# Kernel tuning notes

Hardware: AMD Instinct MI355X
Metric: run time of the kernel (lower is better)

The kernel has to match this reference:

```python
import jax, jax.numpy as jnp
import numpy as np

EMBED_DIM = 768
NUM_HEADS = 12
HEAD_DIM = EMBED_DIM // NUM_HEADS


def setup_inputs() -> dict:
    key = jax.random.key(0)
    k_x, k_wqkv, k_bqkv, k_wo, k_bo = jax.random.split(key, 5)
    B, S = 2, 4096
    x = jax.random.normal(k_x, (B, S, EMBED_DIM), dtype=jnp.float32)
    # nn.Linear default init: U(-1/sqrt(fan_in), 1/sqrt(fan_in))
    bound = 1.0 / np.sqrt(EMBED_DIM)
    w_qkv = jax.random.uniform(k_wqkv, (EMBED_DIM, 3 * EMBED_DIM), jnp.float32, -bound, bound)
    b_qkv = jax.random.uniform(k_bqkv, (3 * EMBED_DIM,), jnp.float32, -bound, bound)
    w_out = jax.random.uniform(k_wo, (EMBED_DIM, EMBED_DIM), jnp.float32, -bound, bound)
    b_out = jax.random.uniform(k_bo, (EMBED_DIM,), jnp.float32, -bound, bound)
    return {"x": x, "w_qkv": w_qkv, "b_qkv": b_qkv, "w_out": w_out, "b_out": b_out}


def reference(x, w_qkv, b_qkv, w_out, b_out):
    B, S, E = x.shape
    H, D = NUM_HEADS, HEAD_DIM
    qkv = x @ w_qkv + b_qkv                       # [B,S,3E]
    qkv = qkv.reshape(B, S, 3, H, D)
    q = qkv[:, :, 0].transpose(0, 2, 1, 3)        # [B,H,S,D]
    k = qkv[:, :, 1].transpose(0, 2, 1, 3)
    v = qkv[:, :, 2].transpose(0, 2, 1, 3)
    scores = jnp.einsum('bhqd,bhkd->bhqk', q, k) / jnp.sqrt(jnp.float32(D))
    causal = jnp.tril(jnp.ones((S, S), dtype=bool))
    scores = jnp.where(causal, scores, -jnp.inf)
    weights = jax.nn.softmax(scores, axis=-1)
    attended = jnp.einsum('bhqk,bhkd->bhqd', weights, v)  # [B,H,S,D]
    attended = attended.transpose(0, 2, 1, 3).reshape(B, S, E)
    return attended @ w_out + b_out
```

## Files before the change

kernel.cpp:

```cpp
#include <hip/hip_runtime.h>

#define EMBED 768
#define NH 12
#define HD 64
#define SEQ 4096
#define BATCH 2
#define MROWS (BATCH * SEQ)
#define N3E (3 * EMBED)

typedef short bf16x8 __attribute__((ext_vector_type(8)));
typedef float fx4 __attribute__((ext_vector_type(4)));
typedef float f32x16 __attribute__((ext_vector_type(16)));
typedef unsigned short ushort_t;
typedef unsigned short us4 __attribute__((ext_vector_type(4)));

#if __has_builtin(__builtin_amdgcn_exp2f)
#define EXP2F(x) __builtin_amdgcn_exp2f(x)
#else
#define EXP2F(x) exp2f(x)
#endif

#define QSCALE 0.18033688011112042f

__device__ inline ushort_t f2bf(float f) {
  union { float f; unsigned int u; } x; x.f = f;
  unsigned int r = x.u + 0x7fffu + ((x.u >> 16) & 1u);
  return (ushort_t)(r >> 16);
}

__device__ inline unsigned int cvtpk(float a, float b) {
  unsigned int r;
  asm("v_cvt_pk_bf16_f32 %0, %1, %2" : "=v"(r) : "v"(a), "v"(b));
  return r;
}

__device__ inline void plswap(unsigned int& x, unsigned int& y) {
  asm("v_permlane32_swap_b32 %0, %1" : "+v"(x), "+v"(y));
}

__global__ __launch_bounds__(256) void convert_x(const float* __restrict__ in,
                                                 ushort_t* __restrict__ out) {
  int i = (blockIdx.x * 256 + threadIdx.x) * 8;
  float4 a = *(const float4*)(in + i);
  float4 b = *(const float4*)(in + i + 4);
  bf16x8 o;
  o[0] = f2bf(a.x); o[1] = f2bf(a.y); o[2] = f2bf(a.z); o[3] = f2bf(a.w);
  o[4] = f2bf(b.x); o[5] = f2bf(b.y); o[6] = f2bf(b.z); o[7] = f2bf(b.w);
  *(bf16x8*)(out + i) = o;
}

__global__ __launch_bounds__(256) void transpose_w(const float* __restrict__ in,
                                                   ushort_t* __restrict__ out,
                                                   int K, int N) {
  __shared__ float t[64][65];
  const int bn = blockIdx.x * 64, bk = blockIdx.y * 64;
  const int c = threadIdx.x & 63, r0 = threadIdx.x >> 6;
#pragma unroll
  for (int rr = 0; rr < 16; ++rr) {
    int row = rr * 4 + r0;
    t[row][c] = in[(size_t)(bk + row) * N + bn + c];
  }
  __syncthreads();
#pragma unroll
  for (int rr = 0; rr < 16; ++rr) {
    int row = rr * 4 + r0;
    out[(size_t)(bn + row) * K + bk + c] = f2bf(t[c][row]);
  }
}

template <int N_, int K_, bool SCATTER>
__global__ __launch_bounds__(256) void gemm_mfma(
    const ushort_t* __restrict__ A, const ushort_t* __restrict__ Bt,
    const float* __restrict__ bias, float* __restrict__ outF,
    ushort_t* __restrict__ oq, ushort_t* __restrict__ ok,
    ushort_t* __restrict__ ov) {
  __shared__ __align__(16) ushort_t As[128 * 32];
  __shared__ __align__(16) ushort_t Bs[128 * 32];
  const int tid = threadIdx.x;
  const int w = tid >> 6, lane = tid & 63;
  const int quad = lane >> 4, ln = lane & 15;
  const int bm = blockIdx.y * 128, bn = blockIdx.x * 128;
  const int wm = (w >> 1) * 64, wn = (w & 1) * 64;

  const int sr = lane >> 2;
  const int sslot = lane & 3;

  fx4 acc[4][4] = {};

  for (int k0 = 0; k0 < K_; k0 += 32) {
    __syncthreads();
#pragma unroll
    for (int r = 0; r < 2; ++r) {
      const int c = w + r * 4;
      const int m = c * 16 + sr;
      const int kk = k0 + ((sslot ^ (m & 3)) << 3);
      __builtin_amdgcn_global_load_lds(
          (const __attribute__((address_space(1))) unsigned int*)
              (A + (size_t)(bm + m) * K_ + kk),
          (__attribute__((address_space(3))) unsigned int*)(As + c * 512),
          16, 0, 0);
      __builtin_amdgcn_global_load_lds(
          (const __attribute__((address_space(1))) unsigned int*)
              (Bt + (size_t)(bn + m) * K_ + kk),
          (__attribute__((address_space(3))) unsigned int*)(Bs + c * 512),
          16, 0, 0);
    }
    __syncthreads();

    bf16x8 af[4], bfr[4];
#pragma unroll
    for (int i = 0; i < 4; ++i) {
      const int m = wm + i * 16 + ln;
      af[i] = *(const bf16x8*)(As + m * 32 + ((quad ^ (m & 3)) << 3));
    }
#pragma unroll
    for (int j = 0; j < 4; ++j) {
      const int n = wn + j * 16 + ln;
      bfr[j] = *(const bf16x8*)(Bs + n * 32 + ((quad ^ (n & 3)) << 3));
    }
#pragma unroll
    for (int i = 0; i < 4; ++i)
#pragma unroll
      for (int j = 0; j < 4; ++j)
        acc[i][j] = __builtin_amdgcn_mfma_f32_16x16x32_bf16(af[i], bfr[j],
                                                            acc[i][j], 0, 0, 0);
  }

  if (!SCATTER) {
#pragma unroll
    for (int j = 0; j < 4; ++j) {
      const int n = bn + wn + j * 16 + ln;
      const float bv = bias[n];
#pragma unroll
      for (int i = 0; i < 4; ++i) {
        const int m0 = bm + wm + i * 16 + quad * 4;
#pragma unroll
        for (int r = 0; r < 4; ++r)
          outF[(size_t)(m0 + r) * N_ + n] = acc[i][j][r] + bv;
      }
    }
  } else {
    const int t = bn / EMBED;
#pragma unroll
    for (int j = 0; j < 4; ++j) {
      const int nn = bn + wn + j * 16 + ln;
      const int rem = nn - t * EMBED;
      const int h = rem >> 6, d = rem & 63;
      const float bv = bias[nn];
#pragma unroll
      for (int i = 0; i < 4; ++i) {
        const int m0 = bm + wm + i * 16 + quad * 4;
#pragma unroll
        for (int r = 0; r < 4; ++r) {
          const int m = m0 + r;
          const int b_ = m >> 12, s = m & 4095;
          const float v = acc[i][j][r] + bv;
          if (t == 0)
            oq[((size_t)(b_ * NH + h) * SEQ + s) * HD + d] = f2bf(v * QSCALE);
          else if (t == 1)
            ok[((size_t)(b_ * NH + h) * SEQ + s) * HD + d] = f2bf(v);
          else
            ov[((size_t)(b_ * NH + h) * HD + d) * SEQ + s] = f2bf(v);
        }
      }
    }
  }
}

__global__ __launch_bounds__(256, 4) void flash_mfma(
    const ushort_t* __restrict__ qb, const ushort_t* __restrict__ kb,
    const ushort_t* __restrict__ vb, ushort_t* __restrict__ attn) {
  __shared__ __align__(16) ushort_t Ks[2][64 * 64];
  __shared__ __align__(16) ushort_t Vt[2][64 * 64];

  const int tid = threadIdx.x;
  const int w = tid >> 6;
  const int lane = tid & 63;
  const int r32 = lane & 31;
  const int hf = lane >> 5;
  const int gk = r32 & 7;
  const int rc4 = hf * 4;

  const int bh = blockIdx.x;
  const int y = blockIdx.y;
  const int qt2 = (y < 11) ? (31 - y) : (y - 11);
  const int ktd0 = 2 * qt2;
  const int nkt = 2 * qt2 + 2;

  const size_t base = (size_t)bh * SEQ * HD;
  const ushort_t* Qg = qb + base;
  const ushort_t* Kg = kb + base;
  const ushort_t* Vg = vb + base;

  const int srow = lane >> 3;
  const int sg = (lane & 7) ^ srow;
  const int row0 = w * 8 + srow;
  const ushort_t* kp = Kg + (size_t)row0 * HD + (sg << 3);
  const ushort_t* vp = Vg + (size_t)row0 * SEQ + (sg << 3);

  const int qoff = w * 32 + r32;
  const int qglob = qt2 * 128 + qoff;
  bf16x8 qf[4];
  {
    const ushort_t* qrow = Qg + (size_t)qglob * HD;
#pragma unroll
    for (int dc = 0; dc < 4; ++dc)
      qf[dc] = *(const bf16x8*)(qrow + dc * 16 + hf * 8);
  }

  f32x16 oacc[2] = {};
  float lsum = 0.f;

#pragma unroll
  for (int r2 = 0; r2 < 2; ++r2) {
    __builtin_amdgcn_global_load_lds(
        (const __attribute__((address_space(1))) unsigned int*)(kp + r2 * (32 * HD)),
        (__attribute__((address_space(3))) unsigned int*)(&Ks[0][(w + r2 * 4) * 512]),
        16, 0, 0);
    __builtin_amdgcn_global_load_lds(
        (const __attribute__((address_space(1))) unsigned int*)(vp + r2 * (32 * SEQ)),
        (__attribute__((address_space(3))) unsigned int*)(&Vt[0][(w + r2 * 4) * 512]),
        16, 0, 0);
  }
  kp += 64 * HD;
  vp += 64;

  for (int kt = 0; kt < nkt; ++kt) {
    const int cur = kt & 1;
    __syncthreads();
    if (kt + 1 < nkt) {
      const int nxt = cur ^ 1;
#pragma unroll
      for (int r2 = 0; r2 < 2; ++r2) {
        __builtin_amdgcn_global_load_lds(
            (const __attribute__((address_space(1))) unsigned int*)(kp + r2 * (32 * HD)),
            (__attribute__((address_space(3))) unsigned int*)(&Ks[nxt][(w + r2 * 4) * 512]),
            16, 0, 0);
        __builtin_amdgcn_global_load_lds(
            (const __attribute__((address_space(1))) unsigned int*)(vp + r2 * (32 * SEQ)),
            (__attribute__((address_space(3))) unsigned int*)(&Vt[nxt][(w + r2 * 4) * 512]),
            16, 0, 0);
      }
      kp += 64 * HD;
      vp += 64;
    }

    const bool diag = (kt >= ktd0);
    const int kbase0 = (kt == ktd0) ? 0 : 64;

#pragma unroll
    for (int krb = 0; krb < 2; ++krb) {
      const int krow = (krb * 32 + r32) * 64;
      f32x16 s = {};
#pragma unroll
      for (int dc = 0; dc < 4; ++dc) {
        bf16x8 kf =
            *(const bf16x8*)(&Ks[cur][krow + (((2 * dc + hf) ^ gk) << 3)]);
        s = __builtin_amdgcn_mfma_f32_32x32x16_bf16(kf, qf[dc], s, 0, 0, 0);
      }
      if (diag) {
        const int kb2 = kbase0 + krb * 32;
#pragma unroll
        for (int r = 0; r < 16; ++r) {
          const int rowc = (r & 3) + 8 * (r >> 2) + rc4;
          if (kb2 + rowc > qoff) s[r] = -1e30f;
        }
      }
      float e[16];
#pragma unroll
      for (int r = 0; r < 16; ++r) {
        e[r] = EXP2F(s[r]);
        lsum += e[r];
      }
#pragma unroll
      for (int ch = 0; ch < 2; ++ch) {
        const int rb = ch * 8;
        unsigned int x0 = cvtpk(e[rb + 0], e[rb + 1]);
        unsigned int x1 = cvtpk(e[rb + 2], e[rb + 3]);
        unsigned int y0 = cvtpk(e[rb + 4], e[rb + 5]);
        unsigned int y1 = cvtpk(e[rb + 6], e[rb + 7]);
        plswap(x0, y0);
        plswap(x1, y1);
        union { unsigned int u[4]; bf16x8 v; } pf;
        pf.u[0] = x0; pf.u[1] = x1; pf.u[2] = y0; pf.u[3] = y1;
        const int c = 2 * krb + ch;
        __builtin_amdgcn_s_setprio(1);
#pragma unroll
        for (int vb2 = 0; vb2 < 2; ++vb2) {
          const int vrow = (vb2 * 32 + r32) * 64;
          bf16x8 vf =
              *(const bf16x8*)(&Vt[cur][vrow + (((2 * c + hf) ^ gk) << 3)]);
          oacc[vb2] =
              __builtin_amdgcn_mfma_f32_32x32x16_bf16(vf, pf.v, oacc[vb2], 0, 0, 0);
        }
        __builtin_amdgcn_s_setprio(0);
      }
    }
  }

  lsum += __shfl_xor(lsum, 32);
  const float inv = 1.f / lsum;
  const int b_ = bh / NH, h = bh % NH;
  ushort_t* orow = attn + (size_t)(b_ * SEQ + qglob) * EMBED + h * HD;
#pragma unroll
  for (int vb2 = 0; vb2 < 2; ++vb2)
#pragma unroll
    for (int rq = 0; rq < 4; ++rq) {
      us4 o;
#pragma unroll
      for (int r = 0; r < 4; ++r) o[r] = f2bf(oacc[vb2][rq * 4 + r] * inv);
      *(us4*)(orow + vb2 * 32 + rq * 8 + rc4) = o;
    }
}

extern "C" void kernel_launch(void* const* d_in, const int* in_sizes, int n_in,
                              void* d_out, int out_size, void* d_ws,
                              size_t ws_size, hipStream_t stream) {
  const float* x = (const float*)d_in[0];
  const float* w_qkv = (const float*)d_in[1];
  const float* b_qkv = (const float*)d_in[2];
  const float* w_out = (const float*)d_in[3];
  const float* b_out = (const float*)d_in[4];
  float* out = (float*)d_out;

  const size_t per = (size_t)BATCH * NH * SEQ * HD;
  ushort_t* q_buf = (ushort_t*)d_ws;
  ushort_t* k_buf = q_buf + per;
  ushort_t* v_buf = k_buf + per;
  ushort_t* attn_buf = v_buf + per;
  ushort_t* xb = attn_buf + per;
  ushort_t* wqkvT = xb + per;
  ushort_t* woutT = wqkvT + (size_t)N3E * EMBED;

  convert_x<<<(MROWS * EMBED) / 2048, 256, 0, stream>>>(x, xb);
  transpose_w<<<dim3(N3E / 64, EMBED / 64), 256, 0, stream>>>(w_qkv, wqkvT,
                                                              EMBED, N3E);
  transpose_w<<<dim3(EMBED / 64, EMBED / 64), 256, 0, stream>>>(w_out, woutT,
                                                                EMBED, EMBED);

  dim3 g1(N3E / 128, MROWS / 128);
  gemm_mfma<N3E, EMBED, true><<<g1, 256, 0, stream>>>(
      xb, wqkvT, b_qkv, nullptr, q_buf, k_buf, v_buf);

  dim3 g2(BATCH * NH, 32);
  flash_mfma<<<g2, 256, 0, stream>>>(q_buf, k_buf, v_buf, attn_buf);

  dim3 g3(EMBED / 128, MROWS / 128);
  gemm_mfma<EMBED, EMBED, false><<<g3, 256, 0, stream>>>(
      attn_buf, woutT, b_out, out, nullptr, nullptr, nullptr);
}
```

Measured before the change: 260.6 us.

## Replace GEMM with 256x256-tile, 8-wave, 4-stage pipelined LDS kernel

Both projection GEMMs move from a 128x128 tile with 4 waves and a single LDS buffer to a 256x256 tile with 8 waves, a 4-deep ring of LDS buffers, and prefetching three k-steps ahead through global_load_lds. Each k-step is split into four MFMA phases. Async loads are interleaved between barriers, and setprio raises wave priority during the MFMA phases. The goal is to hide global-load latency and raise operand reuse per LDS read. The cost is 128KB of LDS per block and far fewer blocks: the output GEMM gets only 96 blocks, and the QKV GEMM 288, which may underfill the CUs.

Measured after the change: 283.6 us. 8.8% more time.

```diff
diff --git a/kernel.cpp b/kernel.cpp
--- a/kernel.cpp
+++ b/kernel.cpp
@@ -10,7 +10,6 @@
 
 typedef short bf16x8 __attribute__((ext_vector_type(8)));
 typedef float fx4 __attribute__((ext_vector_type(4)));
-typedef float f32x16 __attribute__((ext_vector_type(16)));
 typedef unsigned short ushort_t;
 typedef unsigned short us4 __attribute__((ext_vector_type(4)));
 
@@ -26,16 +25,6 @@
   union { float f; unsigned int u; } x; x.f = f;
   unsigned int r = x.u + 0x7fffu + ((x.u >> 16) & 1u);
   return (ushort_t)(r >> 16);
-}
-
-__device__ inline unsigned int cvtpk(float a, float b) {
-  unsigned int r;
-  asm("v_cvt_pk_bf16_f32 %0, %1, %2" : "=v"(r) : "v"(a), "v"(b));
-  return r;
-}
-
-__device__ inline void plswap(unsigned int& x, unsigned int& y) {
-  asm("v_permlane32_swap_b32 %0, %1" : "+v"(x), "+v"(y));
 }
 
 __global__ __launch_bounds__(256) void convert_x(const float* __restrict__ in,
@@ -69,95 +58,169 @@
 }
 
 template <int N_, int K_, bool SCATTER>
-__global__ __launch_bounds__(256) void gemm_mfma(
+__global__ __launch_bounds__(512) void gemm_256(
     const ushort_t* __restrict__ A, const ushort_t* __restrict__ Bt,
     const float* __restrict__ bias, float* __restrict__ outF,
     ushort_t* __restrict__ oq, ushort_t* __restrict__ ok,
     ushort_t* __restrict__ ov) {
-  __shared__ __align__(16) ushort_t As[128 * 32];
-  __shared__ __align__(16) ushort_t Bs[128 * 32];
+  constexpr int NT = K_ / 32;
+  __shared__ __align__(16) ushort_t As[4][256 * 32];
+  __shared__ __align__(16) ushort_t Bs[4][256 * 32];
   const int tid = threadIdx.x;
-  const int w = tid >> 6, lane = tid & 63;
+  const int wid = tid >> 6, lane = tid & 63;
   const int quad = lane >> 4, ln = lane & 15;
-  const int bm = blockIdx.y * 128, bn = blockIdx.x * 128;
-  const int wm = (w >> 1) * 64, wn = (w & 1) * 64;
-
-  const int sr = lane >> 2;
-  const int sslot = lane & 3;
-
-  fx4 acc[4][4] = {};
-
-  for (int k0 = 0; k0 < K_; k0 += 32) {
-    __syncthreads();
-#pragma unroll
-    for (int r = 0; r < 2; ++r) {
-      const int c = w + r * 4;
-      const int m = c * 16 + sr;
-      const int kk = k0 + ((sslot ^ (m & 3)) << 3);
-      __builtin_amdgcn_global_load_lds(
-          (const __attribute__((address_space(1))) unsigned int*)
-              (A + (size_t)(bm + m) * K_ + kk),
-          (__attribute__((address_space(3))) unsigned int*)(As + c * 512),
-          16, 0, 0);
-      __builtin_amdgcn_global_load_lds(
-          (const __attribute__((address_space(1))) unsigned int*)
-              (Bt + (size_t)(bn + m) * K_ + kk),
-          (__attribute__((address_space(3))) unsigned int*)(Bs + c * 512),
-          16, 0, 0);
-    }
-    __syncthreads();
-
-    bf16x8 af[4], bfr[4];
-#pragma unroll
-    for (int i = 0; i < 4; ++i) {
-      const int m = wm + i * 16 + ln;
-      af[i] = *(const bf16x8*)(As + m * 32 + ((quad ^ (m & 3)) << 3));
-    }
+  const int wr = wid >> 2, wc = wid & 3;
+  const int bm = blockIdx.y * 256, bn = blockIdx.x * 256;
+
+  const int srow = lane >> 2;
+  const int sgr = (lane & 3) ^ (srow & 3);
+  const ushort_t* pA[2];
+  const ushort_t* pB[2];
+#pragma unroll
+  for (int a = 0; a < 2; ++a) {
+    pA[a] = A + (size_t)(bm + a * 128 + wid * 16 + srow) * K_ + (sgr << 3);
+    pB[a] = Bt + (size_t)(bn + a * 128 + wid * 16 + srow) * K_ + (sgr << 3);
+  }
+  const int ldst0 = wid * 16 * 32;
+
+  const int abase = (wr * 128 + ln) * 32 + ((quad ^ (ln & 3)) << 3);
+  const int bbase = (wc * 64 + ln) * 32 + ((quad ^ (ln & 3)) << 3);
+
+  fx4 acc[8][4] = {};
+
+#pragma unroll
+  for (int ti = 0; ti < 3; ++ti) {
+#pragma unroll
+    for (int a = 0; a < 2; ++a)
+      __builtin_amdgcn_global_load_lds(
+          (const __attribute__((address_space(1))) unsigned int*)(pA[a] + ti * 32),
+          (__attribute__((address_space(3))) unsigned int*)(&As[ti][a * 4096 + ldst0]),
+          16, 0, 0);
+#pragma unroll
+    for (int b = 0; b < 2; ++b)
+      __builtin_amdgcn_global_load_lds(
+          (const __attribute__((address_space(1))) unsigned int*)(pB[b] + ti * 32),
+          (__attribute__((address_space(3))) unsigned int*)(&Bs[ti][b * 4096 + ldst0]),
+          16, 0, 0);
+  }
+
+#pragma unroll 4
+  for (int t = 0; t < NT; ++t) {
+    const int buf = t & 3;
+    asm volatile("s_waitcnt vmcnt(8)" ::: "memory");
+    __builtin_amdgcn_s_barrier();
+    const ushort_t* Ab = &As[buf][0];
+    const ushort_t* Bb = &Bs[buf][0];
+    const int nbuf = (t + 3) & 3;
+    const bool st = (t + 3) < NT;
+    bf16x8 af[4], b01[2], b23[2];
+
+#pragma unroll
+    for (int i = 0; i < 4; ++i) af[i] = *(const bf16x8*)(Ab + abase + i * 512);
+#pragma unroll
+    for (int j = 0; j < 2; ++j) b01[j] = *(const bf16x8*)(Bb + bbase + j * 512);
+    if (st)
+      __builtin_amdgcn_global_load_lds(
+          (const __attribute__((address_space(1))) unsigned int*)(pA[0] + (t + 3) * 32),
+          (__attribute__((address_space(3))) unsigned int*)(&As[nbuf][ldst0]),
+          16, 0, 0);
+    __builtin_amdgcn_s_barrier();
+    __builtin_amdgcn_s_setprio(1);
+#pragma unroll
+    for (int i = 0; i < 4; ++i)
+#pragma unroll
+      for (int j = 0; j < 2; ++j)
+        acc[i][j] = __builtin_amdgcn_mfma_f32_16x16x32_bf16(af[i], b01[j],
+                                                            acc[i][j], 0, 0, 0);
+    __builtin_amdgcn_s_setprio(0);
+    __builtin_amdgcn_s_barrier();
+
+#pragma unroll
+    for (int j = 0; j < 2; ++j)
+      b23[j] = *(const bf16x8*)(Bb + bbase + (2 + j) * 512);
+    if (st)
+      __builtin_amdgcn_global_load_lds(
+          (const __attribute__((address_space(1))) unsigned int*)(pA[1] + (t + 3) * 32),
+          (__attribute__((address_space(3))) unsigned int*)(&As[nbuf][4096 + ldst0]),
+          16, 0, 0);
+    __builtin_amdgcn_s_barrier();
+    __builtin_amdgcn_s_setprio(1);
+#pragma unroll
+    for (int i = 0; i < 4; ++i)
+#pragma unroll
+      for (int j = 0; j < 2; ++j)
+        acc[i][2 + j] = __builtin_amdgcn_mfma_f32_16x16x32_bf16(
+            af[i], b23[j], acc[i][2 + j], 0, 0, 0);
+    __builtin_amdgcn_s_setprio(0);
+    __builtin_amdgcn_s_barrier();
+
+#pragma unroll
+    for (int i = 0; i < 4; ++i)
+      af[i] = *(const bf16x8*)(Ab + abase + (4 + i) * 512);
+    if (st)
+      __builtin_amdgcn_global_load_lds(
+          (const __attribute__((address_space(1))) unsigned int*)(pB[0] + (t + 3) * 32),
+          (__attribute__((address_space(3))) unsigned int*)(&Bs[nbuf][ldst0]),
+          16, 0, 0);
+    __builtin_amdgcn_s_barrier();
+    __builtin_amdgcn_s_setprio(1);
+#pragma unroll
+    for (int i = 0; i < 4; ++i)
+#pragma unroll
+      for (int j = 0; j < 2; ++j)
+        acc[4 + i][2 + j] = __builtin_amdgcn_mfma_f32_16x16x32_bf16(
+            af[i], b23[j], acc[4 + i][2 + j], 0, 0, 0);
+    __builtin_amdgcn_s_setprio(0);
+    __builtin_amdgcn_s_barrier();
+
+    if (st)
+      __builtin_amdgcn_global_load_lds(
+          (const __attribute__((address_space(1))) unsigned int*)(pB[1] + (t + 3) * 32),
+          (__attribute__((address_space(3))) unsigned int*)(&Bs[nbuf][4096 + ldst0]),
+          16, 0, 0);
+    __builtin_amdgcn_s_barrier();
+    __builtin_amdgcn_s_setprio(1);
+#pragma unroll
+    for (int i = 0; i < 4; ++i)
+#pragma unroll
+      for (int j = 0; j < 2; ++j)
+        acc[4 + i][j] = __builtin_amdgcn_mfma_f32_16x16x32_bf16(
+            af[i], b01[j], acc[4 + i][j], 0, 0, 0);
+    __builtin_amdgcn_s_setprio(0);
+  }
+
+  if (!SCATTER) {
 #pragma unroll
     for (int j = 0; j < 4; ++j) {
-      const int n = wn + j * 16 + ln;
-      bfr[j] = *(const bf16x8*)(Bs + n * 32 + ((quad ^ (n & 3)) << 3));
-    }
-#pragma unroll
-    for (int i = 0; i < 4; ++i)
-#pragma unroll
-      for (int j = 0; j < 4; ++j)
-        acc[i][j] = __builtin_amdgcn_mfma_f32_16x16x32_bf16(af[i], bfr[j],
-                                                            acc[i][j], 0, 0, 0);
-  }
-
-  if (!SCATTER) {
-#pragma unroll
-    for (int j = 0; j < 4; ++j) {
-      const int n = bn + wn + j * 16 + ln;
+      const int n = bn + wc * 64 + j * 16 + ln;
       const float bv = bias[n];
 #pragma unroll
-      for (int i = 0; i < 4; ++i) {
-        const int m0 = bm + wm + i * 16 + quad * 4;
+      for (int i = 0; i < 8; ++i) {
+        const int m0 = bm + wr * 128 + i * 16 + quad * 4;
 #pragma unroll
         for (int r = 0; r < 4; ++r)
           outF[(size_t)(m0 + r) * N_ + n] = acc[i][j][r] + bv;
       }
     }
   } else {
-    const int t = bn / EMBED;
+    const int t3 = bn / EMBED;
 #pragma unroll
     for (int j = 0; j < 4; ++j) {
-      const int nn = bn + wn + j * 16 + ln;
-      const int rem = nn - t * EMBED;
+      const int nn = bn + wc * 64 + j * 16 + ln;
+      const int rem = nn - t3 * EMBED;
       const int h = rem >> 6, d = rem & 63;
       const float bv = bias[nn];
 #pragma unroll
-      for (int i = 0; i < 4; ++i) {
-        const int m0 = bm + wm + i * 16 + quad * 4;
+      for (int i = 0; i < 8; ++i) {
+        const int m0 = bm + wr * 128 + i * 16 + quad * 4;
 #pragma unroll
         for (int r = 0; r < 4; ++r) {
           const int m = m0 + r;
           const int b_ = m >> 12, s = m & 4095;
           const float v = acc[i][j][r] + bv;
-          if (t == 0)
+          if (t3 == 0)
             oq[((size_t)(b_ * NH + h) * SEQ + s) * HD + d] = f2bf(v * QSCALE);
-          else if (t == 1)
+          else if (t3 == 1)
             ok[((size_t)(b_ * NH + h) * SEQ + s) * HD + d] = f2bf(v);
           else
             ov[((size_t)(b_ * NH + h) * HD + d) * SEQ + s] = f2bf(v);
@@ -165,6 +228,17 @@
       }
     }
   }
+}
+
+typedef float f32x16 __attribute__((ext_vector_type(16)));
+
+__device__ inline unsigned int cvtpk(float a, float b) {
+  unsigned int r;
+  asm("v_cvt_pk_bf16_f32 %0, %1, %2" : "=v"(r) : "v"(a), "v"(b));
+  return r;
+}
+__device__ inline void plswap(unsigned int& x, unsigned int& y) {
+  asm("v_permlane32_swap_b32 %0, %1" : "+v"(x), "+v"(y));
 }
 
 __global__ __launch_bounds__(256, 4) void flash_mfma(
@@ -338,14 +412,14 @@
   transpose_w<<<dim3(EMBED / 64, EMBED / 64), 256, 0, stream>>>(w_out, woutT,
                                                                 EMBED, EMBED);
 
-  dim3 g1(N3E / 128, MROWS / 128);
-  gemm_mfma<N3E, EMBED, true><<<g1, 256, 0, stream>>>(
+  dim3 g1(N3E / 256, MROWS / 256);
+  gemm_256<N3E, EMBED, true><<<g1, 512, 0, stream>>>(
       xb, wqkvT, b_qkv, nullptr, q_buf, k_buf, v_buf);
 
   dim3 g2(BATCH * NH, 32);
   flash_mfma<<<g2, 256, 0, stream>>>(q_buf, k_buf, v_buf, attn_buf);
 
-  dim3 g3(EMBED / 128, MROWS / 128);
-  gemm_mfma<EMBED, EMBED, false><<<g3, 256, 0, stream>>>(
+  dim3 g3(EMBED / 256, MROWS / 256);
+  gemm_256<EMBED, EMBED, false><<<g3, 512, 0, stream>>>(
       attn_buf, woutT, b_out, out, nullptr, nullptr, nullptr);
 }
```

## Triple-buffer GEMM LDS loads and remap workgroups for L2 locality

Applied to the files above, without the earlier changes.

The GEMM mainloop now keeps three LDS buffers and issues async global-to-LDS loads two tiles ahead, waiting with vmcnt only on the oldest tile. The old loop needed two barriers per K step and exposed load latency. Workgroup IDs are also remapped in groups of 8, likely to spread or group tiles across XCDs for better L2 reuse. This uses more LDS, which may lower occupancy, and relies on the vmcnt count matching the four loads issued per stage.

Measured after the change: 256.8 us. Within noise of the previous version (-1.4%).

```diff
diff --git a/kernel.cpp b/kernel.cpp
--- a/kernel.cpp
+++ b/kernel.cpp
@@ -33,7 +33,6 @@
   asm("v_cvt_pk_bf16_f32 %0, %1, %2" : "=v"(r) : "v"(a), "v"(b));
   return r;
 }
-
 __device__ inline void plswap(unsigned int& x, unsigned int& y) {
   asm("v_permlane32_swap_b32 %0, %1" : "+v"(x), "+v"(y));
 }
@@ -74,49 +73,55 @@
     const float* __restrict__ bias, float* __restrict__ outF,
     ushort_t* __restrict__ oq, ushort_t* __restrict__ ok,
     ushort_t* __restrict__ ov) {
-  __shared__ __align__(16) ushort_t As[128 * 32];
-  __shared__ __align__(16) ushort_t Bs[128 * 32];
+  constexpr int NT = K_ / 32;
+  __shared__ __align__(16) ushort_t As[3][128 * 32];
+  __shared__ __align__(16) ushort_t Bs[3][128 * 32];
   const int tid = threadIdx.x;
   const int w = tid >> 6, lane = tid & 63;
   const int quad = lane >> 4, ln = lane & 15;
-  const int bm = blockIdx.y * 128, bn = blockIdx.x * 128;
+
+  const int gx = gridDim.x;
+  const int nwg = gx * gridDim.y;
+  int lin = blockIdx.y * gx + blockIdx.x;
+  lin = (lin & 7) * (nwg >> 3) + (lin >> 3);
+  const int bm = (lin / gx) * 128, bn = (lin % gx) * 128;
+
   const int wm = (w >> 1) * 64, wn = (w & 1) * 64;
-
   const int sr = lane >> 2;
   const int sslot = lane & 3;
 
-  fx4 acc[4][4] = {};
-
-  for (int k0 = 0; k0 < K_; k0 += 32) {
-    __syncthreads();
+  auto STAGE = [&](int ti, int b) {
 #pragma unroll
     for (int r = 0; r < 2; ++r) {
       const int c = w + r * 4;
       const int m = c * 16 + sr;
-      const int kk = k0 + ((sslot ^ (m & 3)) << 3);
+      const int kk = ti * 32 + ((sslot ^ (m & 3)) << 3);
       __builtin_amdgcn_global_load_lds(
           (const __attribute__((address_space(1))) unsigned int*)
               (A + (size_t)(bm + m) * K_ + kk),
-          (__attribute__((address_space(3))) unsigned int*)(As + c * 512),
+          (__attribute__((address_space(3))) unsigned int*)(&As[b][c * 512]),
           16, 0, 0);
       __builtin_amdgcn_global_load_lds(
           (const __attribute__((address_space(1))) unsigned int*)
               (Bt + (size_t)(bn + m) * K_ + kk),
-          (__attribute__((address_space(3))) unsigned int*)(Bs + c * 512),
+          (__attribute__((address_space(3))) unsigned int*)(&Bs[b][c * 512]),
           16, 0, 0);
     }
-    __syncthreads();
-
+  };
+
+  fx4 acc[4][4] = {};
+
+  auto COMPUTE = [&](int b) {
     bf16x8 af[4], bfr[4];
 #pragma unroll
     for (int i = 0; i < 4; ++i) {
       const int m = wm + i * 16 + ln;
-      af[i] = *(const bf16x8*)(As + m * 32 + ((quad ^ (m & 3)) << 3));
+      af[i] = *(const bf16x8*)(&As[b][m * 32 + ((quad ^ (m & 3)) << 3)]);
     }
 #pragma unroll
     for (int j = 0; j < 4; ++j) {
       const int n = wn + j * 16 + ln;
-      bfr[j] = *(const bf16x8*)(Bs + n * 32 + ((quad ^ (n & 3)) << 3));
+      bfr[j] = *(const bf16x8*)(&Bs[b][n * 32 + ((quad ^ (n & 3)) << 3)]);
     }
 #pragma unroll
     for (int i = 0; i < 4; ++i)
@@ -124,7 +129,30 @@
       for (int j = 0; j < 4; ++j)
         acc[i][j] = __builtin_amdgcn_mfma_f32_16x16x32_bf16(af[i], bfr[j],
                                                             acc[i][j], 0, 0, 0);
-  }
+  };
+
+  STAGE(0, 0);
+  STAGE(1, 1);
+
+  int bufR = 0;
+  for (int t = 0; t < NT - 2; ++t) {
+    asm volatile("s_waitcnt vmcnt(4)" ::: "memory");
+    __builtin_amdgcn_s_barrier();
+    __builtin_amdgcn_sched_barrier(0);
+    const int bufS = (bufR >= 1) ? bufR - 1 : 2;
+    STAGE(t + 2, bufS);
+    COMPUTE(bufR);
+    bufR = (bufR < 2) ? bufR + 1 : 0;
+  }
+  asm volatile("s_waitcnt vmcnt(4)" ::: "memory");
+  __builtin_amdgcn_s_barrier();
+  __builtin_amdgcn_sched_barrier(0);
+  COMPUTE(bufR);
+  bufR = (bufR < 2) ? bufR + 1 : 0;
+  asm volatile("s_waitcnt vmcnt(0)" ::: "memory");
+  __builtin_amdgcn_s_barrier();
+  __builtin_amdgcn_sched_barrier(0);
+  COMPUTE(bufR);
 
   if (!SCATTER) {
 #pragma unroll
@@ -140,11 +168,11 @@
       }
     }
   } else {
-    const int t = bn / EMBED;
+    const int t3 = bn / EMBED;
 #pragma unroll
     for (int j = 0; j < 4; ++j) {
       const int nn = bn + wn + j * 16 + ln;
-      const int rem = nn - t * EMBED;
+      const int rem = nn - t3 * EMBED;
       const int h = rem >> 6, d = rem & 63;
       const float bv = bias[nn];
 #pragma unroll
@@ -155,9 +183,9 @@
           const int m = m0 + r;
           const int b_ = m >> 12, s = m & 4095;
           const float v = acc[i][j][r] + bv;
-          if (t == 0)
+          if (t3 == 0)
             oq[((size_t)(b_ * NH + h) * SEQ + s) * HD + d] = f2bf(v * QSCALE);
-          else if (t == 1)
+          else if (t3 == 1)
             ok[((size_t)(b_ * NH + h) * SEQ + s) * HD + d] = f2bf(v);
           else
             ov[((size_t)(b_ * NH + h) * HD + d) * SEQ + s] = f2bf(v);
```
